# Kernel optimization log

Hardware: AMD Instinct MI355X
Metric: run time of the kernel (lower is better)

Reference implementation:

```python
import jax, jax.numpy as jnp
import numpy as np

S = 2          # scale_int = ceil(scale)
K = 3          # kernel size
OUTC = 3       # num_out_ch
NUM_FEAT = 64


def conv3x3(x, w, b):
    y = jax.lax.conv_general_dilated(x, w, (1, 1), ((1, 1), (1, 1)),
                                     dimension_numbers=('NCHW', 'OIHW', 'NCHW'))
    return y + b[None, :, None, None]


def unfold3x3(x):
    # torch F.unfold(x, 3, padding=1): (N, C*9, H*W), order c*9 + ki*3 + kj
    N, C, H, W = x.shape
    xp = jnp.pad(x, ((0, 0), (0, 0), (1, 1), (1, 1)))
    patches = jnp.stack([xp[:, :, i:i + H, j:j + W]
                         for i in range(3) for j in range(3)], axis=2)  # (N,C,9,H,W)
    return patches.reshape(N, C * 9, H * W)


def setup_inputs() -> dict:
    key = jax.random.key(0)
    ks = jax.random.split(key, 12)
    b, t, c, h, w = 2, 4, 16, 64, 64
    H, W = S * h, S * w
    nf4 = 64 // 4  # 16
    d_w = K * K * NUM_FEAT * OUTC  # 1728
    return {
        'x0': jax.random.normal(ks[0], (b, NUM_FEAT, h, w), jnp.float32),
        'feature': jax.random.normal(ks[1], (b, t, c, h, w), jnp.float32),
        'pos_mat': jax.random.uniform(ks[2], (H, W, 3), jnp.float32),
        'mask': jnp.ones((b, OUTC, H, W), dtype=bool),
        'conv1_w': jax.random.normal(ks[3], (nf4, 64, 3, 3), jnp.float32) * 0.05,
        'conv1_b': jnp.zeros((nf4,), jnp.float32),
        'conv2_w': jax.random.normal(ks[4], (nf4, nf4, 3, 3), jnp.float32) * 0.05,
        'conv2_b': jnp.zeros((nf4,), jnp.float32),
        'f2w1_w': jax.random.normal(ks[5], (256, nf4 + 1), jnp.float32) * 0.05,
        'f2w1_b': jnp.zeros((256,), jnp.float32),
        'f2w2_w': jax.random.normal(ks[6], (d_w, 256), jnp.float32) * 0.05,
        'f2w2_b': jnp.zeros((d_w,), jnp.float32),
    }


def reference(x0, feature, pos_mat, mask, conv1_w, conv1_b, conv2_w, conv2_b,
              f2w1_w, f2w1_b, f2w2_w, f2w2_b):
    b, t, c, h, w = feature.shape
    H, W = S * h, S * w
    # with_gradBack=False -> feature.detach()
    feat = jax.lax.stop_gradient(feature).reshape(b, t * c, h, w)
    # repeat_x(..., upsample=True): nearest-neighbour upsample by S
    feat_up = jnp.repeat(jnp.repeat(feat, S, axis=2), S, axis=3)  # (b,64,H,W)
    f = jax.nn.relu(conv3x3(feat_up, conv1_w, conv1_b))
    f = conv3x3(f, conv2_w, conv2_b)                              # (b,16,H,W)
    pos0 = jnp.transpose(pos_mat, (2, 0, 1))[0:1]                 # (1,H,W)
    fm = jnp.concatenate([f, jnp.broadcast_to(pos0[None], (b, 1, H, W))], axis=1)
    fm = fm.reshape(b, -1, H * W).transpose(0, 2, 1)              # (b,HW,17)
    hdn = jax.nn.relu(fm @ f2w1_w.T + f2w1_b)
    weights = hdn @ f2w2_w.T + f2w2_b                             # (b,HW,1728)
    weights = weights.reshape(b, h, S, w, S, K * K * NUM_FEAT, OUTC)
    weights = jnp.transpose(weights, (0, 2, 4, 1, 3, 5, 6))
    weights = weights.reshape(b, S * S, h * w, K * K * NUM_FEAT, OUTC)
    # repeat_x(x0) tiles x0 S^2 times -> all S^2 col copies identical; compute once
    cols = unfold3x3(x0).transpose(0, 2, 1)                       # (b,hw,576)
    out = jnp.einsum('bpk,bspko->bspo', cols, weights)            # (b,S^2,hw,3)
    out = jnp.transpose(out, (0, 1, 3, 2)).reshape(b, S, S, OUTC, h, w)
    out = jnp.transpose(out, (0, 3, 4, 1, 5, 2)).reshape(b, OUTC, H, W)
    # integer scale -> mask all True -> masked_select + view is identity
    return out, weights
```

## Files before the change

### kernel.cpp

```cpp
#include <hip/hip_runtime.h>

#define THREADS 256

#define Bsz 2
#define HWp 16384
#define Ntot (Bsz*HWp)
#define HID 256
#define Mm 1728
#define FMC 17
#define W_OFF 98304

#define F1_OFF  0
#define F1_SZ   (Bsz*16*HWp)
#define FM_OFF  F1_SZ
#define WB2_OFF (FM_OFF + Ntot*FMC)
#define WB1_OFF (WB2_OFF + (Mm*HID)/2)

typedef __attribute__((ext_vector_type(8))) short bf16x8;
typedef __attribute__((ext_vector_type(4))) float f32x4;

static __device__ __forceinline__ short f2bf(float x) {
    unsigned u = __builtin_bit_cast(unsigned, x);
    unsigned r = (u + 0x7fff + ((u >> 16) & 1)) >> 16;
    return (short)r;
}

__global__ __launch_bounds__(THREADS) void k13_conv1_cvt(const float* __restrict__ feat,
                                                         const float* __restrict__ w1,
                                                         const float* __restrict__ b1,
                                                         float* __restrict__ f1,
                                                         const float* __restrict__ w2g,
                                                         short* __restrict__ wB2,
                                                         const float* __restrict__ w1g,
                                                         short* __restrict__ wB1) {
    int tid = threadIdx.x;
    if (blockIdx.x >= 1984) {
        for (int idx = tid; idx < 8192; idx += THREADS) {
            int i = idx & 7, l = (idx >> 3) & 63, h = idx >> 9;
            int k = (l >> 4) * 8 + i, hid = h * 16 + (l & 15);
            wB1[idx] = (k < FMC) ? f2bf(w1g[hid * FMC + k]) : (short)0;
        }
        return;
    }
    if (blockIdx.x >= 256) {
        int t = (blockIdx.x - 256) * THREADS + tid;
        int i = t & 7, l = (t >> 3) & 63, ct = (t >> 9) & 3, s = (t >> 11) & 7, mc = t >> 14;
        int col = mc * 64 + ct * 16 + (l & 15);
        int k = s * 32 + (l >> 4) * 8 + i;
        wB2[t] = f2bf(w2g[col * HID + k]);
        return;
    }
    __shared__ float sW[4 * 64 * 4];
    int b = blockIdx.x;
    int rb = b & 7, oc = (b >> 3) & 15, bb = b >> 7;
    int c = tid & 63, sr = tid >> 6;
    int r0 = rb * 4 + sr;
    int r1 = r0 + 32;

    #pragma unroll
    for (int q = 0; q < 4; ++q) {
        int e = tid * 4 + q;
        int v = e & 1, u = (e >> 1) & 1, ic = (e >> 2) & 63, pp = (e >> 8) & 3;
        int pi = pp >> 1, pj = pp & 1;
        float s = 0.f;
        for (int ki = 0; ki < 3; ++ki) {
            bool okki = pi ? (u ? (ki == 2) : (ki <= 1)) : (u ? (ki >= 1) : (ki == 0));
            if (!okki) continue;
            for (int kj = 0; kj < 3; ++kj) {
                bool okkj = pj ? (v ? (kj == 2) : (kj <= 1)) : (v ? (kj >= 1) : (kj == 0));
                if (okkj) s += w1[((oc * 64 + ic) * 3 + ki) * 3 + kj];
            }
        }
        sW[(pp * 64 + ic) * 4 + u * 2 + v] = s;
    }
    __syncthreads();

    float bias = b1[oc];
    float aA00 = bias, aA01 = bias, aA10 = bias, aA11 = bias;
    float aB00 = bias, aB01 = bias, aB10 = bias, aB11 = bias;

    float mA = (r0 > 0) ? 1.f : 0.f;
    float mB = (r1 < 63) ? 1.f : 0.f;
    float mc0 = (c > 0) ? 1.f : 0.f, mc2 = (c < 63) ? 1.f : 0.f;
    int roA0 = (r0 > 0) ? -64 : 0;
    int roB2 = (r1 < 63) ? 64 : 0;
    int co0 = (c > 0) ? -1 : 0, co2 = (c < 63) ? 1 : 0;

    const float* fbA = feat + bb * 64 * 4096 + r0 * 64 + c;
    const float* fbB = feat + bb * 64 * 4096 + r1 * 64 + c;
    for (int ic = 0; ic < 64; ++ic) {
        const float* pA1 = fbA + ic * 4096;
        const float* pA0 = pA1 + roA0;
        const float* pA2 = pA1 + 64;
        const float* pB1 = fbB + ic * 4096;
        const float* pB0 = pB1 - 64;
        const float* pB2 = pB1 + roB2;

        float vA00 = pA0[co0] * (mA * mc0), vA01 = pA0[0] * mA, vA02 = pA0[co2] * (mA * mc2);
        float vA10 = pA1[co0] * mc0,        vA11 = pA1[0],      vA12 = pA1[co2] * mc2;
        float vA20 = pA2[co0] * mc0,        vA21 = pA2[0],      vA22 = pA2[co2] * mc2;
        float vB00 = pB0[co0] * mc0,        vB01 = pB0[0],      vB02 = pB0[co2] * mc2;
        float vB10 = pB1[co0] * mc0,        vB11 = pB1[0],      vB12 = pB1[co2] * mc2;
        float vB20 = pB2[co0] * (mB * mc0), vB21 = pB2[0] * mB, vB22 = pB2[co2] * (mB * mc2);

        f32x4 w0 = *(const f32x4*)(sW + (0 * 64 + ic) * 4);
        f32x4 w1v = *(const f32x4*)(sW + (1 * 64 + ic) * 4);
        f32x4 w2v = *(const f32x4*)(sW + (2 * 64 + ic) * 4);
        f32x4 w3 = *(const f32x4*)(sW + (3 * 64 + ic) * 4);

        aA00 = fmaf(w0[0], vA00, aA00); aA00 = fmaf(w0[1], vA01, aA00);
        aA00 = fmaf(w0[2], vA10, aA00); aA00 = fmaf(w0[3], vA11, aA00);
        aA01 = fmaf(w1v[0], vA01, aA01); aA01 = fmaf(w1v[1], vA02, aA01);
        aA01 = fmaf(w1v[2], vA11, aA01); aA01 = fmaf(w1v[3], vA12, aA01);
        aA10 = fmaf(w2v[0], vA10, aA10); aA10 = fmaf(w2v[1], vA11, aA10);
        aA10 = fmaf(w2v[2], vA20, aA10); aA10 = fmaf(w2v[3], vA21, aA10);
        aA11 = fmaf(w3[0], vA11, aA11); aA11 = fmaf(w3[1], vA12, aA11);
        aA11 = fmaf(w3[2], vA21, aA11); aA11 = fmaf(w3[3], vA22, aA11);

        aB00 = fmaf(w0[0], vB00, aB00); aB00 = fmaf(w0[1], vB01, aB00);
        aB00 = fmaf(w0[2], vB10, aB00); aB00 = fmaf(w0[3], vB11, aB00);
        aB01 = fmaf(w1v[0], vB01, aB01); aB01 = fmaf(w1v[1], vB02, aB01);
        aB01 = fmaf(w1v[2], vB11, aB01); aB01 = fmaf(w1v[3], vB12, aB01);
        aB10 = fmaf(w2v[0], vB10, aB10); aB10 = fmaf(w2v[1], vB11, aB10);
        aB10 = fmaf(w2v[2], vB20, aB10); aB10 = fmaf(w2v[3], vB21, aB10);
        aB11 = fmaf(w3[0], vB11, aB11); aB11 = fmaf(w3[1], vB12, aB11);
        aB11 = fmaf(w3[2], vB21, aB11); aB11 = fmaf(w3[3], vB22, aB11);
    }

    float* foA = f1 + (bb * 16 + oc) * HWp + (2 * r0) * 128 + 2 * c;
    *reinterpret_cast<float2*>(foA)       = make_float2(fmaxf(aA00, 0.f), fmaxf(aA01, 0.f));
    *reinterpret_cast<float2*>(foA + 128) = make_float2(fmaxf(aA10, 0.f), fmaxf(aA11, 0.f));
    float* foB = f1 + (bb * 16 + oc) * HWp + (2 * r1) * 128 + 2 * c;
    *reinterpret_cast<float2*>(foB)       = make_float2(fmaxf(aB00, 0.f), fmaxf(aB01, 0.f));
    *reinterpret_cast<float2*>(foB + 128) = make_float2(fmaxf(aB10, 0.f), fmaxf(aB11, 0.f));
}

__global__ __launch_bounds__(THREADS) void k2_conv2_fm(const float* __restrict__ f1,
                                                       const float* __restrict__ w2,
                                                       const float* __restrict__ b2,
                                                       const float* __restrict__ pos,
                                                       float* __restrict__ fm) {
    int tid = threadIdx.x;
    int t = blockIdx.x * THREADS + tid;
    int J = t & 127, I = (t >> 7) & 127, h = (t >> 14) & 1, bb = t >> 15;

    float acc[8];
    #pragma unroll
    for (int o = 0; o < 8; ++o) acc[o] = b2[h * 8 + o];

    int ro0 = (I > 0) ? -128 : 0, ro2 = (I < 127) ? 128 : 0;
    int co0 = (J > 0) ? -1 : 0, co2 = (J < 127) ? 1 : 0;
    float mr0 = (I > 0) ? 1.f : 0.f, mr2 = (I < 127) ? 1.f : 0.f;
    float mcl = (J > 0) ? 1.f : 0.f, mcr = (J < 127) ? 1.f : 0.f;

    const float* fb = f1 + bb * 16 * HWp + I * 128 + J;
    #pragma unroll 4
    for (int ic = 0; ic < 16; ++ic) {
        const float* p1 = fb + ic * HWp;
        const float* p0 = p1 + ro0;
        const float* p2 = p1 + ro2;
        float v0 = p0[co0] * (mr0 * mcl), v1 = p0[0] * mr0, v2 = p0[co2] * (mr0 * mcr);
        float v3 = p1[co0] * mcl,         v4 = p1[0],       v5 = p1[co2] * mcr;
        float v6 = p2[co0] * (mr2 * mcl), v7 = p2[0] * mr2, v8 = p2[co2] * (mr2 * mcr);
        const float* wp = w2 + (h * 8 * 16 + ic) * 9;
        #pragma unroll
        for (int o = 0; o < 8; ++o) {
            const float* w = wp + o * 144;
            acc[o] = fmaf(v0, w[0], acc[o]); acc[o] = fmaf(v1, w[1], acc[o]);
            acc[o] = fmaf(v2, w[2], acc[o]); acc[o] = fmaf(v3, w[3], acc[o]);
            acc[o] = fmaf(v4, w[4], acc[o]); acc[o] = fmaf(v5, w[5], acc[o]);
            acc[o] = fmaf(v6, w[6], acc[o]); acc[o] = fmaf(v7, w[7], acc[o]);
            acc[o] = fmaf(v8, w[8], acc[o]);
        }
    }
    int n = bb * HWp + I * 128 + J;
    #pragma unroll
    for (int o = 0; o < 8; ++o) fm[n * FMC + h * 8 + o] = acc[o];
    if (h == 0) fm[n * FMC + 16] = pos[(I * 128 + J) * 3];
}

__global__ __launch_bounds__(THREADS) void k35_hdn(const float* __restrict__ fm,
                                                   const short* __restrict__ wB1,
                                                   const float* __restrict__ b1g,
                                                   float* __restrict__ dout) {
    int tid = threadIdx.x;
    int n0 = blockIdx.x * 64;
    int bb = n0 >> 14, tt = n0 & 16383, I = tt >> 7, J0 = tt & 127;
    int s0 = (I & 1) * 2, i0 = I >> 1, jmin = J0 >> 1;
    short* sp = (short*)(dout + (size_t)W_OFF +
                         ((size_t)(bb * 4 + s0) * 4096 + i0 * 64 + jmin) * Mm);

    int w = tid >> 6, l = tid & 63, lm = l & 15, lg = l >> 4;
    int row = w * 16 + lm;
    const float* fr = fm + (n0 + row) * FMC;
    bf16x8 af;
    #pragma unroll
    for (int i = 0; i < 8; ++i) {
        int k = lg * 8 + i;
        float x = (k < FMC) ? fr[k] : 0.f;
        af[i] = f2bf(x);
    }
    const short* wb = wB1 + l * 8;
    int pbase = ((lg >> 1) * 64 + row) * 8 + (lg & 1) * 4;
    #pragma unroll 4
    for (int h = 0; h < 16; ++h) {
        bf16x8 bfr = *(const bf16x8*)(wb + h * 512);
        f32x4 bias = *(const f32x4*)(b1g + h * 16 + lg * 4);
        f32x4 acc = __builtin_amdgcn_mfma_f32_16x16x32_bf16(bfr, af, bias, 0, 0, 0);
        unsigned c0 = (unsigned short)f2bf(fmaxf(acc[0], 0.f));
        unsigned c1 = (unsigned short)f2bf(fmaxf(acc[1], 0.f));
        unsigned c2 = (unsigned short)f2bf(fmaxf(acc[2], 0.f));
        unsigned c3 = (unsigned short)f2bf(fmaxf(acc[3], 0.f));
        uint2 uv; uv.x = c0 | (c1 << 16); uv.y = c2 | (c3 << 16);
        *(uint2*)(sp + pbase + h * 1024) = uv;
    }
}

__global__ __launch_bounds__(THREADS, 2) void k4_gemm(const short* __restrict__ wB2,
                                                      const float* __restrict__ b2g,
                                                      const float* __restrict__ x0g,
                                                      float* __restrict__ dout) {
    __shared__ short sA[16384];
    __shared__ int   sOB[64];
    __shared__ float sXT[6632];
    __shared__ float sOut[4 * 64 * 3];

    int tid = threadIdx.x;
    int n0 = blockIdx.x * 64;
    int bb = n0 >> 14, tt = n0 & 16383, I = tt >> 7, J0 = tt & 127;
    int s0 = (I & 1) * 2, i0 = I >> 1, jmin = J0 >> 1;

    {
        const short* spc = (const short*)(dout + (size_t)W_OFF +
                             ((size_t)(bb * 4 + s0) * 4096 + i0 * 64 + jmin) * Mm);
        #pragma unroll
        for (int q = 0; q < 8; ++q) {
            int si = (q * 256 + tid) * 8;
            *(bf16x8*)(sA + si) = *(const bf16x8*)(spc + si);
        }
    }
    if (tid < 64) {
        int J = J0 + tid;
        int s = ((I & 1) << 1) | (J & 1);
        int p = ((I >> 1) << 6) | (J >> 1);
        sOB[tid] = W_OFF + ((bb * 4 + s) * 4096 + p) * Mm;
    }
    {
        const float* x0b = x0g + bb * 64 * 4096;
        for (int e = tid; e < 6528; e += THREADS) {
            int ch = e / 102, r2 = e - ch * 102;
            int ki = r2 / 34, jc = r2 - ki * 34;
            int y = i0 + ki - 1, x = jmin + jc - 1;
            float v = 0.f;
            if ((unsigned)y < 64u && (unsigned)x < 64u) v = x0b[(ch * 64 + y) * 64 + x];
            sXT[jc * 195 + ch * 3 + ki] = v;
        }
    }
    __syncthreads();

    int wid = tid >> 6, l = tid & 63;
    int lm = l & 15, lg = l >> 4;
    int lg3 = lg % 3, lg4 = lg * 4;

    int pixbase[4], jl195[4];
    #pragma unroll
    for (int rt = 0; rt < 4; ++rt) {
        pixbase[rt] = sOB[rt * 16 + lm];
        jl195[rt] = (rt * 8 + (lm >> 1)) * 195;
    }

    const short* aptr = sA + lg * 512 + lm * 8;

    float racc[4][3];
    #pragma unroll
    for (int rt = 0; rt < 4; ++rt) {
        racc[rt][0] = 0.f; racc[rt][1] = 0.f; racc[rt][2] = 0.f;
    }

    for (int mc = wid; mc < 27; mc += 4) {
        int m0 = mc * 64;
        f32x4 acc[4][4];
        #pragma unroll
        for (int ct = 0; ct < 4; ++ct) {
            f32x4 bias4 = *(const f32x4*)(b2g + m0 + ct * 16 + lg * 4);
            #pragma unroll
            for (int rt = 0; rt < 4; ++rt)
                acc[rt][ct] = bias4;
        }
        const short* bbase = wB2 + (size_t)mc * 16384 + l * 8;
        #pragma unroll 2
        for (int s = 0; s < 8; ++s) {
            bf16x8 af[4], bfr[4];
            #pragma unroll
            for (int rt = 0; rt < 4; ++rt)
                af[rt] = *(const bf16x8*)(aptr + s * 2048 + rt * 128);
            #pragma unroll
            for (int ct = 0; ct < 4; ++ct)
                bfr[ct] = *(const bf16x8*)(bbase + (s * 4 + ct) * 512);
            #pragma unroll
            for (int rt = 0; rt < 4; ++rt)
                #pragma unroll
                for (int ct = 0; ct < 4; ++ct)
                    acc[rt][ct] = __builtin_amdgcn_mfma_f32_16x16x32_bf16(
                        bfr[ct], af[rt], acc[rt][ct], 0, 0, 0);
        }
        #pragma unroll
        for (int rt = 0; rt < 4; ++rt)
            #pragma unroll
            for (int ct = 0; ct < 4; ++ct)
                *(f32x4*)(dout + pixbase[rt] + m0 + ct * 16 + lg * 4) = acc[rt][ct];
#define ACCUM(QB)                                                              \
        _Pragma("unroll")                                                      \
        for (int ct = 0; ct < 4; ++ct) {                                       \
            int t = m0 + ct * 16 + lg4;                                        \
            int K0 = (t * 21846) >> 16;                                        \
            int rem3 = t - 3 * K0;                                             \
            int Q2 = (K0 * 21846) >> 16;                                       \
            int kja = K0 - 3 * Q2;                                             \
            int kqa = kja * 195 + Q2;                                          \
            int kqb = (kja == 2) ? (Q2 + 1) : (kqa + 195);                     \
            _Pragma("unroll")                                                  \
            for (int rt = 0; rt < 4; ++rt) {                                   \
                float xa = sXT[jl195[rt] + kqa];                               \
                float xb = sXT[jl195[rt] + kqb];                               \
                float x1 = (rem3 == 2) ? xb : xa;                              \
                float x2 = (rem3 >= 1) ? xb : xa;                              \
                racc[rt][(QB + ct) % 3] =                                      \
                    fmaf(acc[rt][ct][0], xa, racc[rt][(QB + ct) % 3]);         \
                racc[rt][(QB + ct + 1) % 3] =                                  \
                    fmaf(acc[rt][ct][1], x1, racc[rt][(QB + ct + 1) % 3]);     \
                racc[rt][(QB + ct + 2) % 3] =                                  \
                    fmaf(acc[rt][ct][2], x2, racc[rt][(QB + ct + 2) % 3]);     \
                racc[rt][(QB + ct) % 3] =                                      \
                    fmaf(acc[rt][ct][3], xb, racc[rt][(QB + ct) % 3]);         \
            }                                                                  \
        }
        switch (mc % 3) {
            case 0: ACCUM(0); break;
            case 1: ACCUM(1); break;
            default: ACCUM(2); break;
        }
#undef ACCUM
    }

    #pragma unroll
    for (int rt = 0; rt < 4; ++rt) {
        float q0 = racc[rt][0], q1 = racc[rt][1], q2 = racc[rt][2];
        float a0 = (lg3 == 0) ? q0 : ((lg3 == 1) ? q2 : q1);
        float a1 = (lg3 == 0) ? q1 : ((lg3 == 1) ? q0 : q2);
        float a2 = (lg3 == 0) ? q2 : ((lg3 == 1) ? q1 : q0);
        a0 += __shfl_xor(a0, 16, 64); a0 += __shfl_xor(a0, 32, 64);
        a1 += __shfl_xor(a1, 16, 64); a1 += __shfl_xor(a1, 32, 64);
        a2 += __shfl_xor(a2, 16, 64); a2 += __shfl_xor(a2, 32, 64);
        if (l < 16) {
            float* so = sOut + (wid * 64 + rt * 16 + lm) * 3;
            so[0] = a0; so[1] = a1; so[2] = a2;
        }
    }
    __syncthreads();
    if (tid < 192) {
        float s = sOut[tid] + sOut[192 + tid] + sOut[384 + tid] + sOut[576 + tid];
        int pix = tid / 3, o = tid - 3 * pix;
        dout[bb * 3 * HWp + o * HWp + I * 128 + J0 + pix] = s;
    }
}

extern "C" void kernel_launch(void* const* d_in, const int* in_sizes, int n_in,
                              void* d_out, int out_size, void* d_ws, size_t ws_size,
                              hipStream_t stream) {
    const float* x0      = (const float*)d_in[0];
    const float* feature = (const float*)d_in[1];
    const float* pos     = (const float*)d_in[2];
    const float* w1      = (const float*)d_in[4];
    const float* b1      = (const float*)d_in[5];
    const float* w2      = (const float*)d_in[6];
    const float* b2      = (const float*)d_in[7];
    const float* f2w1_w  = (const float*)d_in[8];
    const float* f2w1_b  = (const float*)d_in[9];
    const float* f2w2_w  = (const float*)d_in[10];
    const float* f2w2_b  = (const float*)d_in[11];

    float* out = (float*)d_out;
    float* ws  = (float*)d_ws;
    float* f1  = ws + F1_OFF;
    float* fm  = ws + FM_OFF;
    short* wB2 = (short*)(ws + WB2_OFF);
    short* wB1 = (short*)(ws + WB1_OFF);

    k13_conv1_cvt<<<1985, THREADS, 0, stream>>>(feature, w1, b1, f1, f2w2_w, wB2,
                                                f2w1_w, wB1);
    k2_conv2_fm<<<(Bsz * 2 * HWp) / THREADS, THREADS, 0, stream>>>(f1, w2, b2, pos, fm);
    k35_hdn<<<Ntot / 64, THREADS, 0, stream>>>(fm, wB1, f2w1_b, out);
    k4_gemm<<<Ntot / 64, THREADS, 0, stream>>>(wB2, f2w2_b, x0, out);
}
```

Measured before the change: 126.5 us.

## Fuse conv2 into hidden-layer kernel via shared-memory halo tiles; vectorize weight conversion

Removes the separate conv2 kernel. Each hidden-layer block now loads a 16-channel, 3-row halo tile of the conv1 output into shared memory, computes conv2 plus the position channel into a shared buffer, and feeds that straight to the MFMA. This drops one launch and the global round trip of the fm intermediate. The conv1 part is re-split so each thread handles one row instead of two, giving twice as many blocks, and the bf16 weight conversion now uses float4 loads and short4 stores. In exchange, the fused blocks redo halo-row loads and read conv2 weights straight from global memory inside the hidden kernel.

```diff
diff --git a/kernel.cpp b/kernel.cpp
--- a/kernel.cpp
+++ b/kernel.cpp
@@ -34,7 +34,7 @@
                                                          const float* __restrict__ w1g,
                                                          short* __restrict__ wB1) {
     int tid = threadIdx.x;
-    if (blockIdx.x >= 1984) {
+    if (blockIdx.x >= 944) {
         for (int idx = tid; idx < 8192; idx += THREADS) {
             int i = idx & 7, l = (idx >> 3) & 63, h = idx >> 9;
             int k = (l >> 4) * 8 + i, hid = h * 16 + (l & 15);
@@ -42,20 +42,21 @@
         }
         return;
     }
-    if (blockIdx.x >= 256) {
-        int t = (blockIdx.x - 256) * THREADS + tid;
-        int i = t & 7, l = (t >> 3) & 63, ct = (t >> 9) & 3, s = (t >> 11) & 7, mc = t >> 14;
+    if (blockIdx.x >= 512) {
+        int t4 = ((blockIdx.x - 512) * THREADS + tid) * 4;
+        int i = t4 & 7, l = (t4 >> 3) & 63, ct = (t4 >> 9) & 3, s = (t4 >> 11) & 7, mc = t4 >> 14;
         int col = mc * 64 + ct * 16 + (l & 15);
-        int k = s * 32 + (l >> 4) * 8 + i;
-        wB2[t] = f2bf(w2g[col * HID + k]);
+        int k0 = s * 32 + (l >> 4) * 8 + i;
+        f32x4 w = *(const f32x4*)(w2g + col * HID + k0);
+        short4 o;
+        o.x = f2bf(w[0]); o.y = f2bf(w[1]); o.z = f2bf(w[2]); o.w = f2bf(w[3]);
+        *(short4*)(wB2 + t4) = o;
         return;
     }
     __shared__ float sW[4 * 64 * 4];
     int b = blockIdx.x;
-    int rb = b & 7, oc = (b >> 3) & 15, bb = b >> 7;
-    int c = tid & 63, sr = tid >> 6;
-    int r0 = rb * 4 + sr;
-    int r1 = r0 + 32;
+    int rg = b & 15, oc = (b >> 4) & 15, bb = b >> 8;
+    int c = tid & 63, r = rg * 4 + (tid >> 6);
 
     #pragma unroll
     for (int q = 0; q < 4; ++q) {
@@ -76,130 +77,105 @@
     __syncthreads();
 
     float bias = b1[oc];
-    float aA00 = bias, aA01 = bias, aA10 = bias, aA11 = bias;
-    float aB00 = bias, aB01 = bias, aB10 = bias, aB11 = bias;
-
-    float mA = (r0 > 0) ? 1.f : 0.f;
-    float mB = (r1 < 63) ? 1.f : 0.f;
-    float mc0 = (c > 0) ? 1.f : 0.f, mc2 = (c < 63) ? 1.f : 0.f;
-    int roA0 = (r0 > 0) ? -64 : 0;
-    int roB2 = (r1 < 63) ? 64 : 0;
+    float a00 = bias, a01 = bias, a10 = bias, a11 = bias;
+
+    float mt = (r > 0) ? 1.f : 0.f, mb2 = (r < 63) ? 1.f : 0.f;
+    float ml = (c > 0) ? 1.f : 0.f, mr2 = (c < 63) ? 1.f : 0.f;
+    int ro0 = (r > 0) ? -64 : 0, ro2 = (r < 63) ? 64 : 0;
     int co0 = (c > 0) ? -1 : 0, co2 = (c < 63) ? 1 : 0;
 
-    const float* fbA = feat + bb * 64 * 4096 + r0 * 64 + c;
-    const float* fbB = feat + bb * 64 * 4096 + r1 * 64 + c;
+    const float* fb = feat + bb * 64 * 4096 + r * 64 + c;
     for (int ic = 0; ic < 64; ++ic) {
-        const float* pA1 = fbA + ic * 4096;
-        const float* pA0 = pA1 + roA0;
-        const float* pA2 = pA1 + 64;
-        const float* pB1 = fbB + ic * 4096;
-        const float* pB0 = pB1 - 64;
-        const float* pB2 = pB1 + roB2;
-
-        float vA00 = pA0[co0] * (mA * mc0), vA01 = pA0[0] * mA, vA02 = pA0[co2] * (mA * mc2);
-        float vA10 = pA1[co0] * mc0,        vA11 = pA1[0],      vA12 = pA1[co2] * mc2;
-        float vA20 = pA2[co0] * mc0,        vA21 = pA2[0],      vA22 = pA2[co2] * mc2;
-        float vB00 = pB0[co0] * mc0,        vB01 = pB0[0],      vB02 = pB0[co2] * mc2;
-        float vB10 = pB1[co0] * mc0,        vB11 = pB1[0],      vB12 = pB1[co2] * mc2;
-        float vB20 = pB2[co0] * (mB * mc0), vB21 = pB2[0] * mB, vB22 = pB2[co2] * (mB * mc2);
+        const float* p1 = fb + ic * 4096;
+        const float* p0 = p1 + ro0;
+        const float* p2 = p1 + ro2;
+        float v00 = p0[co0] * (mt * ml), v01 = p0[0] * mt, v02 = p0[co2] * (mt * mr2);
+        float v10 = p1[co0] * ml,        v11 = p1[0],      v12 = p1[co2] * mr2;
+        float v20 = p2[co0] * (mb2 * ml), v21 = p2[0] * mb2, v22 = p2[co2] * (mb2 * mr2);
 
         f32x4 w0 = *(const f32x4*)(sW + (0 * 64 + ic) * 4);
         f32x4 w1v = *(const f32x4*)(sW + (1 * 64 + ic) * 4);
         f32x4 w2v = *(const f32x4*)(sW + (2 * 64 + ic) * 4);
         f32x4 w3 = *(const f32x4*)(sW + (3 * 64 + ic) * 4);
 
-        aA00 = fmaf(w0[0], vA00, aA00); aA00 = fmaf(w0[1], vA01, aA00);
-        aA00 = fmaf(w0[2], vA10, aA00); aA00 = fmaf(w0[3], vA11, aA00);
-        aA01 = fmaf(w1v[0], vA01, aA01); aA01 = fmaf(w1v[1], vA02, aA01);
-        aA01 = fmaf(w1v[2], vA11, aA01); aA01 = fmaf(w1v[3], vA12, aA01);
-        aA10 = fmaf(w2v[0], vA10, aA10); aA10 = fmaf(w2v[1], vA11, aA10);
-        aA10 = fmaf(w2v[2], vA20, aA10); aA10 = fmaf(w2v[3], vA21, aA10);
-        aA11 = fmaf(w3[0], vA11, aA11); aA11 = fmaf(w3[1], vA12, aA11);
-        aA11 = fmaf(w3[2], vA21, aA11); aA11 = fmaf(w3[3], vA22, aA11);
-
-        aB00 = fmaf(w0[0], vB00, aB00); aB00 = fmaf(w0[1], vB01, aB00);
-        aB00 = fmaf(w0[2], vB10, aB00); aB00 = fmaf(w0[3], vB11, aB00);
-        aB01 = fmaf(w1v[0], vB01, aB01); aB01 = fmaf(w1v[1], vB02, aB01);
-        aB01 = fmaf(w1v[2], vB11, aB01); aB01 = fmaf(w1v[3], vB12, aB01);
-        aB10 = fmaf(w2v[0], vB10, aB10); aB10 = fmaf(w2v[1], vB11, aB10);
-        aB10 = fmaf(w2v[2], vB20, aB10); aB10 = fmaf(w2v[3], vB21, aB10);
-        aB11 = fmaf(w3[0], vB11, aB11); aB11 = fmaf(w3[1], vB12, aB11);
-        aB11 = fmaf(w3[2], vB21, aB11); aB11 = fmaf(w3[3], vB22, aB11);
-    }
-
-    float* foA = f1 + (bb * 16 + oc) * HWp + (2 * r0) * 128 + 2 * c;
-    *reinterpret_cast<float2*>(foA)       = make_float2(fmaxf(aA00, 0.f), fmaxf(aA01, 0.f));
-    *reinterpret_cast<float2*>(foA + 128) = make_float2(fmaxf(aA10, 0.f), fmaxf(aA11, 0.f));
-    float* foB = f1 + (bb * 16 + oc) * HWp + (2 * r1) * 128 + 2 * c;
-    *reinterpret_cast<float2*>(foB)       = make_float2(fmaxf(aB00, 0.f), fmaxf(aB01, 0.f));
-    *reinterpret_cast<float2*>(foB + 128) = make_float2(fmaxf(aB10, 0.f), fmaxf(aB11, 0.f));
-}
-
-__global__ __launch_bounds__(THREADS) void k2_conv2_fm(const float* __restrict__ f1,
-                                                       const float* __restrict__ w2,
-                                                       const float* __restrict__ b2,
-                                                       const float* __restrict__ pos,
-                                                       float* __restrict__ fm) {
-    int tid = threadIdx.x;
-    int t = blockIdx.x * THREADS + tid;
-    int J = t & 127, I = (t >> 7) & 127, h = (t >> 14) & 1, bb = t >> 15;
-
-    float acc[8];
-    #pragma unroll
-    for (int o = 0; o < 8; ++o) acc[o] = b2[h * 8 + o];
-
-    int ro0 = (I > 0) ? -128 : 0, ro2 = (I < 127) ? 128 : 0;
-    int co0 = (J > 0) ? -1 : 0, co2 = (J < 127) ? 1 : 0;
-    float mr0 = (I > 0) ? 1.f : 0.f, mr2 = (I < 127) ? 1.f : 0.f;
-    float mcl = (J > 0) ? 1.f : 0.f, mcr = (J < 127) ? 1.f : 0.f;
-
-    const float* fb = f1 + bb * 16 * HWp + I * 128 + J;
-    #pragma unroll 4
-    for (int ic = 0; ic < 16; ++ic) {
-        const float* p1 = fb + ic * HWp;
-        const float* p0 = p1 + ro0;
-        const float* p2 = p1 + ro2;
-        float v0 = p0[co0] * (mr0 * mcl), v1 = p0[0] * mr0, v2 = p0[co2] * (mr0 * mcr);
-        float v3 = p1[co0] * mcl,         v4 = p1[0],       v5 = p1[co2] * mcr;
-        float v6 = p2[co0] * (mr2 * mcl), v7 = p2[0] * mr2, v8 = p2[co2] * (mr2 * mcr);
-        const float* wp = w2 + (h * 8 * 16 + ic) * 9;
-        #pragma unroll
-        for (int o = 0; o < 8; ++o) {
-            const float* w = wp + o * 144;
-            acc[o] = fmaf(v0, w[0], acc[o]); acc[o] = fmaf(v1, w[1], acc[o]);
-            acc[o] = fmaf(v2, w[2], acc[o]); acc[o] = fmaf(v3, w[3], acc[o]);
-            acc[o] = fmaf(v4, w[4], acc[o]); acc[o] = fmaf(v5, w[5], acc[o]);
-            acc[o] = fmaf(v6, w[6], acc[o]); acc[o] = fmaf(v7, w[7], acc[o]);
-            acc[o] = fmaf(v8, w[8], acc[o]);
-        }
-    }
-    int n = bb * HWp + I * 128 + J;
-    #pragma unroll
-    for (int o = 0; o < 8; ++o) fm[n * FMC + h * 8 + o] = acc[o];
-    if (h == 0) fm[n * FMC + 16] = pos[(I * 128 + J) * 3];
-}
-
-__global__ __launch_bounds__(THREADS) void k35_hdn(const float* __restrict__ fm,
+        a00 = fmaf(w0[0], v00, a00); a00 = fmaf(w0[1], v01, a00);
+        a00 = fmaf(w0[2], v10, a00); a00 = fmaf(w0[3], v11, a00);
+        a01 = fmaf(w1v[0], v01, a01); a01 = fmaf(w1v[1], v02, a01);
+        a01 = fmaf(w1v[2], v11, a01); a01 = fmaf(w1v[3], v12, a01);
+        a10 = fmaf(w2v[0], v10, a10); a10 = fmaf(w2v[1], v11, a10);
+        a10 = fmaf(w2v[2], v20, a10); a10 = fmaf(w2v[3], v21, a10);
+        a11 = fmaf(w3[0], v11, a11); a11 = fmaf(w3[1], v12, a11);
+        a11 = fmaf(w3[2], v21, a11); a11 = fmaf(w3[3], v22, a11);
+    }
+
+    float* fo = f1 + (bb * 16 + oc) * HWp + (2 * r) * 128 + 2 * c;
+    *reinterpret_cast<float2*>(fo)       = make_float2(fmaxf(a00, 0.f), fmaxf(a01, 0.f));
+    *reinterpret_cast<float2*>(fo + 128) = make_float2(fmaxf(a10, 0.f), fmaxf(a11, 0.f));
+}
+
+__global__ __launch_bounds__(THREADS) void k35_hdn(const float* __restrict__ f1,
+                                                   const float* __restrict__ w2,
+                                                   const float* __restrict__ b2,
+                                                   const float* __restrict__ pos,
                                                    const short* __restrict__ wB1,
                                                    const float* __restrict__ b1g,
                                                    float* __restrict__ dout) {
+    __shared__ float sF[16 * 3 * 68];
+    __shared__ float sFM[64 * 33];
     int tid = threadIdx.x;
     int n0 = blockIdx.x * 64;
     int bb = n0 >> 14, tt = n0 & 16383, I = tt >> 7, J0 = tt & 127;
+
+    for (int e = tid; e < 16 * 3 * 68; e += THREADS) {
+        int jc = e % 68, r2 = e / 68;
+        int di = r2 % 3, ic = r2 / 3;
+        int y = I + di - 1, x = J0 + jc - 1;
+        float v = 0.f;
+        if ((unsigned)y < 128u && (unsigned)x < 128u && jc < 66)
+            v = f1[(bb * 16 + ic) * HWp + y * 128 + x];
+        sF[(ic * 3 + di) * 68 + jc] = v;
+    }
+    for (int e = tid; e < 64 * 33; e += THREADS) sFM[e] = 0.f;
+    __syncthreads();
+
+    {
+        int pix = tid & 63, q = tid >> 6;
+        float acc[4];
+        #pragma unroll
+        for (int o = 0; o < 4; ++o) acc[o] = b2[q * 4 + o];
+        #pragma unroll 4
+        for (int ic = 0; ic < 16; ++ic) {
+            float v[9];
+            #pragma unroll
+            for (int di = 0; di < 3; ++di) {
+                const float* row = sF + (ic * 3 + di) * 68 + pix;
+                v[di * 3 + 0] = row[0]; v[di * 3 + 1] = row[1]; v[di * 3 + 2] = row[2];
+            }
+            #pragma unroll
+            for (int o = 0; o < 4; ++o) {
+                const float* w = w2 + ((q * 4 + o) * 16 + ic) * 9;
+                acc[o] = fmaf(v[0], w[0], acc[o]); acc[o] = fmaf(v[1], w[1], acc[o]);
+                acc[o] = fmaf(v[2], w[2], acc[o]); acc[o] = fmaf(v[3], w[3], acc[o]);
+                acc[o] = fmaf(v[4], w[4], acc[o]); acc[o] = fmaf(v[5], w[5], acc[o]);
+                acc[o] = fmaf(v[6], w[6], acc[o]); acc[o] = fmaf(v[7], w[7], acc[o]);
+                acc[o] = fmaf(v[8], w[8], acc[o]);
+            }
+        }
+        #pragma unroll
+        for (int o = 0; o < 4; ++o) sFM[pix * 33 + q * 4 + o] = acc[o];
+        if (q == 0) sFM[pix * 33 + 16] = pos[(I * 128 + J0 + pix) * 3];
+    }
+    __syncthreads();
+
+    int w = tid >> 6, l = tid & 63, lm = l & 15, lg = l >> 4;
+    int row = w * 16 + lm;
+    bf16x8 af;
+    #pragma unroll
+    for (int i = 0; i < 8; ++i) af[i] = f2bf(sFM[row * 33 + lg * 8 + i]);
+
     int s0 = (I & 1) * 2, i0 = I >> 1, jmin = J0 >> 1;
     short* sp = (short*)(dout + (size_t)W_OFF +
                          ((size_t)(bb * 4 + s0) * 4096 + i0 * 64 + jmin) * Mm);
-
-    int w = tid >> 6, l = tid & 63, lm = l & 15, lg = l >> 4;
-    int row = w * 16 + lm;
-    const float* fr = fm + (n0 + row) * FMC;
-    bf16x8 af;
-    #pragma unroll
-    for (int i = 0; i < 8; ++i) {
-        int k = lg * 8 + i;
-        float x = (k < FMC) ? fr[k] : 0.f;
-        af[i] = f2bf(x);
-    }
     const short* wb = wB1 + l * 8;
     int pbase = ((lg >> 1) * 64 + row) * 8 + (lg & 1) * 4;
     #pragma unroll 4
@@ -383,13 +359,11 @@
     float* out = (float*)d_out;
     float* ws  = (float*)d_ws;
     float* f1  = ws + F1_OFF;
-    float* fm  = ws + FM_OFF;
     short* wB2 = (short*)(ws + WB2_OFF);
     short* wB1 = (short*)(ws + WB1_OFF);
 
-    k13_conv1_cvt<<<1985, THREADS, 0, stream>>>(feature, w1, b1, f1, f2w2_w, wB2,
-                                                f2w1_w, wB1);
-    k2_conv2_fm<<<(Bsz * 2 * HWp) / THREADS, THREADS, 0, stream>>>(f1, w2, b2, pos, fm);
-    k35_hdn<<<Ntot / 64, THREADS, 0, stream>>>(fm, wB1, f2w1_b, out);
+    k13_conv1_cvt<<<945, THREADS, 0, stream>>>(feature, w1, b1, f1, f2w2_w, wB2,
+                                               f2w1_w, wB1);
+    k35_hdn<<<Ntot / 64, THREADS, 0, stream>>>(f1, w2, b2, pos, wB1, f2w1_b, out);
     k4_gemm<<<Ntot / 64, THREADS, 0, stream>>>(wB2, f2w2_b, x0, out);
 }
```

Result: faster. 112.5 us (-11.1%).
